# Optimization experiments

Hardware: AMD Instinct MI355X
Metric: run time of the kernel (lower is better)

The kernel has to match this reference:

```python
import jax, jax.numpy as jnp
import numpy as np

N, D, T = 4096, 256, 8
RHO = 16.0
DT = 1.0 / T


def setup_inputs() -> dict:
    key = jax.random.key(0)
    k1, k2, k3, k4 = jax.random.split(key, 4)
    X = jax.random.normal(k1, (N, D), dtype=jnp.float32)
    # learned deformation parameters (small init so the Euler flow stays stable)
    A = jax.random.normal(k2, (T, N, D), dtype=jnp.float32) * 0.01
    A_aff = jax.random.normal(k3, (T, D, D), dtype=jnp.float32) * 0.01
    b_aff = jax.random.normal(k4, (T, D), dtype=jnp.float32) * 0.01
    return {"X": X, "A": A, "A_aff": A_aff, "b_aff": b_aff}


def _flow(X, A, A_aff, b_aff):
    inv_two_rho2 = 1.0 / (2.0 * RHO * RHO)

    def step(Z, params_t):
        A_t, Aaff_t, baff_t = params_t
        # Gaussian self-kernel K[i,j] = exp(-||z_i - z_j||^2 / (2 rho^2))
        sq = jnp.sum(Z * Z, axis=1)                      # [n]
        dist = sq[:, None] + sq[None, :] - 2.0 * (Z @ Z.T)  # [n, n]
        K = jnp.exp(-dist * inv_two_rho2)
        # velocity: affine part + RKHS (kernel message aggregation) part
        v = Z @ Aaff_t.T + baff_t[None, :] + K @ A_t     # [n, d]
        return Z + DT * v, None

    Z_final, _ = jax.lax.scan(step, X, (A, A_aff, b_aff))
    return Z_final


def reference(X, A, A_aff, b_aff):
    return _flow(X, A, A_aff, b_aff)
```

## Files before the change

kernel.cpp:

```cpp
#include <hip/hip_runtime.h>


#define N_PTS 4096
#define DIM   256
#define DT_C  0.125f
#define C1    (1.0f/512.0f)

typedef __bf16 bf16x8 __attribute__((ext_vector_type(8)));
typedef float  f32x16 __attribute__((ext_vector_type(16)));
typedef float  f32x4v __attribute__((ext_vector_type(4)));
typedef unsigned int   u32x4 __attribute__((ext_vector_type(4)));
typedef unsigned short u16x8 __attribute__((ext_vector_type(8)));

__device__ __forceinline__ unsigned short f2bf(float f) {
  unsigned int u = __builtin_bit_cast(unsigned int, f);
  u += 0x7fffu + ((u >> 16) & 1u);
  return (unsigned short)(u >> 16);
}
__device__ __forceinline__ float bf2f(unsigned short s) {
  unsigned int u = ((unsigned int)s) << 16;
  return __builtin_bit_cast(float, u);
}

__global__ __launch_bounds__(256) void k_prep(const float* __restrict__ A,
                                              unsigned short* __restrict__ ATf) {
  __shared__ float sT[64][36];
  const int jgrp = blockIdx.x, ds = blockIdx.y, t = blockIdx.z;
  const int tid = threadIdx.x;
  const float* Ab = A + (size_t)t * N_PTS * DIM;
  {
    const int j_l = tid >> 2, dq = tid & 3;
    const float* src = Ab + (size_t)(jgrp * 64 + j_l) * DIM + ds * 32 + dq * 8;
    f32x4v v0 = *(const f32x4v*)src, v1 = *(const f32x4v*)(src + 4);
    *(f32x4v*)&sT[j_l][dq * 8] = v0;
    *(f32x4v*)&sT[j_l][dq * 8 + 4] = v1;
  }
  __syncthreads();
  const int jb_l = tid >> 6, l = tid & 63, l31 = l & 31, lhi = l >> 5;
  u16x8 o;
#pragma unroll
  for (int e = 0; e < 8; ++e) o[e] = f2bf(sT[jb_l * 16 + lhi * 8 + e][l31]);
  unsigned short* dst = ATf + (size_t)t * (8 * 256 * 64 * 8)
                      + ((size_t)(ds * 256 + jgrp * 4 + jb_l) * 64 + l) * 8;
  *(u16x8*)dst = o;
}

__global__ __launch_bounds__(256) void k_init(const float* __restrict__ X,
                                              unsigned short* __restrict__ Zf,
                                              float* __restrict__ erow) {
  const int tid = threadIdx.x;
  const int r = blockIdx.x * 8 + (tid >> 5), o = tid & 31;
  const size_t base = (size_t)r * DIM + o * 8;
  f32x4v z0 = *(const f32x4v*)(X + base), z1 = *(const f32x4v*)(X + base + 4);
  u16x8 zb; float s = 0.f;
#pragma unroll
  for (int i = 0; i < 4; ++i) { zb[i] = f2bf(z0[i]); zb[4 + i] = f2bf(z1[i]);
                                s += z0[i] * z0[i] + z1[i] * z1[i]; }
  *(u16x8*)(Zf + ((size_t)((r >> 5) * 16 + (o >> 1)) * 64 + (o & 1) * 32 + (r & 31)) * 8) = zb;
#pragma unroll
  for (int d = 16; d > 0; d >>= 1) s += __shfl_down(s, d, 32);
  if (o == 0) erow[r] = __expf(-s * C1);
}

__global__ __launch_bounds__(512, 4) void k_flash(
    const unsigned short* __restrict__ Zf, const float* __restrict__ erow,
    const unsigned short* __restrict__ ATf_t,
    const float* __restrict__ Aaff_t,
    unsigned short* __restrict__ Opart) {
  __shared__ __align__(16) unsigned short sZi[64 * 256];
  __shared__ __align__(16) unsigned short sP[2][64 * 64];

  const int tid = threadIdx.x, lane = tid & 63, wid = tid >> 6;
  const int l31 = lane & 31, lhi = lane >> 5;
  const int chunk = blockIdx.x;
  const int i0 = blockIdx.y * 64;
  const int ib = i0 >> 5;

  {
    const unsigned short* src = Zf + (size_t)ib * 8192;
#pragma unroll
    for (int p = 0; p < 4; ++p)
      *(u32x4*)(sZi + (size_t)(p * 512 + tid) * 8) =
          *(const u32x4*)(src + (size_t)(p * 512 + tid) * 8);
  }
  __syncthreads();

  if (wid < 4) {
    const int ip = wid >> 1, jh = wid & 1;
    float eI[16];
#pragma unroll
    for (int c = 0; c < 16; ++c)
      eI[c] = erow[i0 + ip * 32 + 4 * lhi + (c & 3) + 8 * (c >> 2)];

    for (int n = 0; n < 8; ++n) {
      u32x4 bv[16];
      {
        const unsigned short* bp =
            Zf + ((size_t)(chunk * 16 + n * 2 + jh) * 16 * 64 + lane) * 8;
#pragma unroll
        for (int ks = 0; ks < 16; ++ks) bv[ks] = *(const u32x4*)(bp + ks * 512);
      }
      f32x16 S;
#pragma unroll
      for (int i = 0; i < 16; ++i) S[i] = 0.f;
#pragma unroll
      for (int ks = 0; ks < 16; ++ks) {
        bf16x8 af = *(const bf16x8*)(sZi + ((size_t)(ip * 16 + ks) * 64 + lane) * 8);
        S = __builtin_amdgcn_mfma_f32_32x32x16_bf16(af, __builtin_bit_cast(bf16x8, bv[ks]), S, 0, 0, 0);
      }
      const float ej = erow[chunk * 512 + n * 64 + jh * 32 + l31];
      unsigned short* pb = sP[n & 1];
      const int blk = jh * 4 + (l31 >> 3), cl = l31 & 7;
#pragma unroll
      for (int c = 0; c < 16; ++c) {
        const int row = ip * 32 + 4 * lhi + (c & 3) + 8 * (c >> 2);
        pb[row * 64 + ((blk ^ (row & 7)) * 8) + cl] =
            f2bf(eI[c] * ej * __expf(2.f * C1 * S[c]));
      }
      __syncthreads();
    }
    __syncthreads();
  } else {
    const int cd = wid - 4;
    f32x16 O[2][2];
#pragma unroll
    for (int rs = 0; rs < 2; ++rs)
#pragma unroll
      for (int ct = 0; ct < 2; ++ct)
#pragma unroll
        for (int i = 0; i < 16; ++i) O[rs][ct][i] = 0.f;

#pragma unroll
    for (int q = 0; q < 2; ++q) {
      const int ksg = chunk * 2 + q;
      bf16x8 a[2];
#pragma unroll
      for (int rs = 0; rs < 2; ++rs)
        a[rs] = *(const bf16x8*)(sZi + ((size_t)(rs * 16 + ksg) * 64 + lane) * 8);
#pragma unroll
      for (int ct = 0; ct < 2; ++ct) {
        const int d = cd * 64 + ct * 32 + l31;
        const float* bp = Aaff_t + (size_t)d * DIM + ksg * 16 + lhi * 8;
        f32x4v f0 = *(const f32x4v*)bp, f1 = *(const f32x4v*)(bp + 4);
        u16x8 tb;
#pragma unroll
        for (int i = 0; i < 4; ++i) { tb[i] = f2bf(f0[i]); tb[4 + i] = f2bf(f1[i]); }
        bf16x8 bv = __builtin_bit_cast(bf16x8, tb);
#pragma unroll
        for (int rs = 0; rs < 2; ++rs)
          O[rs][ct] = __builtin_amdgcn_mfma_f32_32x32x16_bf16(a[rs], bv, O[rs][ct], 0, 0, 0);
      }
    }
    __syncthreads();

    for (int n = 1; n <= 8; ++n) {
      const int m = n - 1;
      u32x4 bw[8];
#pragma unroll
      for (int ks = 0; ks < 4; ++ks)
#pragma unroll
        for (int ct = 0; ct < 2; ++ct)
          bw[ks * 2 + ct] = *(const u32x4*)(ATf_t +
              ((size_t)((cd * 2 + ct) * 256 + chunk * 32 + m * 4 + ks) * 64 + lane) * 8);
      const unsigned short* pb = sP[m & 1];
#pragma unroll
      for (int ks = 0; ks < 4; ++ks) {
        bf16x8 a[2];
        const int blk = ks * 2 + lhi;
#pragma unroll
        for (int rs = 0; rs < 2; ++rs) {
          const int row = rs * 32 + l31;
          a[rs] = *(const bf16x8*)&pb[row * 64 + ((blk ^ (row & 7)) * 8)];
        }
#pragma unroll
        for (int rs = 0; rs < 2; ++rs)
#pragma unroll
          for (int ct = 0; ct < 2; ++ct)
            O[rs][ct] = __builtin_amdgcn_mfma_f32_32x32x16_bf16(
                a[rs], __builtin_bit_cast(bf16x8, bw[ks * 2 + ct]), O[rs][ct], 0, 0, 0);
      }
      __syncthreads();
    }

    unsigned short* ob = Opart + (size_t)chunk * N_PTS * DIM + (size_t)cd * 64 + l31;
#pragma unroll
    for (int rs = 0; rs < 2; ++rs)
#pragma unroll
      for (int c = 0; c < 16; ++c) {
        const int row = i0 + rs * 32 + 4 * lhi + (c & 3) + 8 * (c >> 2);
        ob[(size_t)row * DIM]      = f2bf(O[rs][0][c]);
        ob[(size_t)row * DIM + 32] = f2bf(O[rs][1][c]);
      }
  }
}

__global__ __launch_bounds__(256) void k_update(const float* __restrict__ Zin,
                                                const unsigned short* __restrict__ Opart,
                                                const float* __restrict__ baff_t,
                                                float* __restrict__ Zout,
                                                unsigned short* __restrict__ Zf,
                                                float* __restrict__ erow) {
  const int tid = threadIdx.x;
  const int r = blockIdx.x * 8 + (tid >> 5), o = tid & 31;
  const size_t base = (size_t)r * DIM + o * 8;
  f32x4v z0 = *(const f32x4v*)(Zin + base), z1 = *(const f32x4v*)(Zin + base + 4);
  f32x4v s0 = *(const f32x4v*)(baff_t + o * 8), s1 = *(const f32x4v*)(baff_t + o * 8 + 4);
#pragma unroll
  for (int c = 0; c < 8; ++c) {
    u16x8 p = *(const u16x8*)(Opart + (size_t)c * N_PTS * DIM + base);
#pragma unroll
    for (int i = 0; i < 4; ++i) { s0[i] += bf2f(p[i]); s1[i] += bf2f(p[4 + i]); }
  }
  u16x8 zb; float sv = 0.f;
#pragma unroll
  for (int i = 0; i < 4; ++i) {
    z0[i] += DT_C * s0[i]; z1[i] += DT_C * s1[i];
    zb[i] = f2bf(z0[i]); zb[4 + i] = f2bf(z1[i]);
    sv += z0[i] * z0[i] + z1[i] * z1[i];
  }
  *(f32x4v*)(Zout + base) = z0;
  *(f32x4v*)(Zout + base + 4) = z1;
  *(u16x8*)(Zf + ((size_t)((r >> 5) * 16 + (o >> 1)) * 64 + (o & 1) * 32 + (r & 31)) * 8) = zb;
#pragma unroll
  for (int d = 16; d > 0; d >>= 1) sv += __shfl_down(sv, d, 32);
  if (o == 0) erow[r] = __expf(-sv * C1);
}

extern "C" void kernel_launch(void* const* d_in, const int* in_sizes, int n_in,
                              void* d_out, int out_size, void* d_ws, size_t ws_size,
                              hipStream_t stream) {
  const float* X    = (const float*)d_in[0];
  const float* A    = (const float*)d_in[1];
  const float* Aaff = (const float*)d_in[2];
  const float* baff = (const float*)d_in[3];
  float* out = (float*)d_out;

  char* w = (char*)d_ws;
  size_t off = 0;
  unsigned short* ATf = (unsigned short*)(w + off); off += (size_t)8 * 8 * 256 * 64 * 8 * 2;
  unsigned short* Zf  = (unsigned short*)(w + off); off += (size_t)N_PTS * DIM * 2;
  float* erow = (float*)(w + off); off += (size_t)N_PTS * 4;
  float* Zf32 = (float*)(w + off); off += (size_t)N_PTS * DIM * 4;
  unsigned short* Opart = (unsigned short*)(w + off); off += (size_t)8 * N_PTS * DIM * 2;
  (void)ws_size; (void)in_sizes; (void)n_in; (void)out_size;

  k_prep<<<dim3(64, 8, 8), 256, 0, stream>>>(A, ATf);
  k_init<<<512, 256, 0, stream>>>(X, Zf, erow);

  const float* zin = X;
  for (int t = 0; t < 8; ++t) {
    float* zout = (t == 7) ? out : Zf32;
    k_flash<<<dim3(8, 64), 512, 0, stream>>>(
        Zf, erow, ATf + (size_t)t * (8 * 256 * 64 * 8), Aaff + (size_t)t * DIM * DIM, Opart);
    k_update<<<512, 256, 0, stream>>>(zin, Opart, baff + (size_t)t * DIM, zout, Zf, erow);
    zin = zout;
  }
}
```

Measured before the change: 381.0 us.

## Shrink flash blocks to 32 rows with one producer and two consumer waves

Reworks k_flash from 64-row tiles with 8 waves (4 producing kernel tiles, 4 accumulating) to 32-row tiles with 3 waves: one wave builds the 32x64 P tile and two waves each accumulate 128 output columns. The grid doubles to 1024 blocks and shared memory per block roughly halves, aiming for more resident blocks and better load balance across CUs. The trade-off is that each j-tile of Z and each ATf tile is reloaded by twice as many blocks. The single producer wave also serializes the S computation, so the pipeline between producer and consumers may become imbalanced.

```diff
diff --git a/kernel.cpp b/kernel.cpp
--- a/kernel.cpp
+++ b/kernel.cpp
@@ -62,134 +62,129 @@
   if (o == 0) erow[r] = __expf(-s * C1);
 }
 
-__global__ __launch_bounds__(512, 4) void k_flash(
+__global__ __launch_bounds__(192, 4) void k_flash(
     const unsigned short* __restrict__ Zf, const float* __restrict__ erow,
     const unsigned short* __restrict__ ATf_t,
     const float* __restrict__ Aaff_t,
     unsigned short* __restrict__ Opart) {
-  __shared__ __align__(16) unsigned short sZi[64 * 256];
-  __shared__ __align__(16) unsigned short sP[2][64 * 64];
+  __shared__ __align__(16) unsigned short sZi[16 * 64 * 8];
+  __shared__ __align__(16) unsigned short sP[2][32 * 64];
 
   const int tid = threadIdx.x, lane = tid & 63, wid = tid >> 6;
   const int l31 = lane & 31, lhi = lane >> 5;
   const int chunk = blockIdx.x;
-  const int i0 = blockIdx.y * 64;
-  const int ib = i0 >> 5;
+  const int iblk = blockIdx.y;
+  const int i0 = iblk * 32;
 
   {
-    const unsigned short* src = Zf + (size_t)ib * 8192;
-#pragma unroll
-    for (int p = 0; p < 4; ++p)
-      *(u32x4*)(sZi + (size_t)(p * 512 + tid) * 8) =
-          *(const u32x4*)(src + (size_t)(p * 512 + tid) * 8);
+    const unsigned short* src = Zf + (size_t)iblk * 8192;
+#pragma unroll
+    for (int p = 0; p < 6; ++p) {
+      int idx = p * 192 + tid;
+      if (idx < 1024)
+        *(u32x4*)(sZi + (size_t)idx * 8) = *(const u32x4*)(src + (size_t)idx * 8);
+    }
   }
   __syncthreads();
 
-  if (wid < 4) {
-    const int ip = wid >> 1, jh = wid & 1;
+  if (wid == 0) {
     float eI[16];
 #pragma unroll
     for (int c = 0; c < 16; ++c)
-      eI[c] = erow[i0 + ip * 32 + 4 * lhi + (c & 3) + 8 * (c >> 2)];
+      eI[c] = erow[i0 + 4 * lhi + (c & 3) + 8 * (c >> 2)];
 
     for (int n = 0; n < 8; ++n) {
-      u32x4 bv[16];
-      {
-        const unsigned short* bp =
-            Zf + ((size_t)(chunk * 16 + n * 2 + jh) * 16 * 64 + lane) * 8;
-#pragma unroll
-        for (int ks = 0; ks < 16; ++ks) bv[ks] = *(const u32x4*)(bp + ks * 512);
-      }
-      f32x16 S;
-#pragma unroll
-      for (int i = 0; i < 16; ++i) S[i] = 0.f;
-#pragma unroll
-      for (int ks = 0; ks < 16; ++ks) {
-        bf16x8 af = *(const bf16x8*)(sZi + ((size_t)(ip * 16 + ks) * 64 + lane) * 8);
-        S = __builtin_amdgcn_mfma_f32_32x32x16_bf16(af, __builtin_bit_cast(bf16x8, bv[ks]), S, 0, 0, 0);
-      }
-      const float ej = erow[chunk * 512 + n * 64 + jh * 32 + l31];
       unsigned short* pb = sP[n & 1];
-      const int blk = jh * 4 + (l31 >> 3), cl = l31 & 7;
-#pragma unroll
-      for (int c = 0; c < 16; ++c) {
-        const int row = ip * 32 + 4 * lhi + (c & 3) + 8 * (c >> 2);
-        pb[row * 64 + ((blk ^ (row & 7)) * 8) + cl] =
-            f2bf(eI[c] * ej * __expf(2.f * C1 * S[c]));
+#pragma unroll
+      for (int jh = 0; jh < 2; ++jh) {
+        u32x4 bv[16];
+        {
+          const unsigned short* bp =
+              Zf + ((size_t)(chunk * 16 + n * 2 + jh) * 16 * 64 + lane) * 8;
+#pragma unroll
+          for (int ks = 0; ks < 16; ++ks) bv[ks] = *(const u32x4*)(bp + ks * 512);
+        }
+        f32x16 S;
+#pragma unroll
+        for (int i = 0; i < 16; ++i) S[i] = 0.f;
+#pragma unroll
+        for (int ks = 0; ks < 16; ++ks) {
+          bf16x8 af = *(const bf16x8*)(sZi + ((size_t)ks * 64 + lane) * 8);
+          S = __builtin_amdgcn_mfma_f32_32x32x16_bf16(
+              af, __builtin_bit_cast(bf16x8, bv[ks]), S, 0, 0, 0);
+        }
+        const float ej = erow[chunk * 512 + n * 64 + jh * 32 + l31];
+        const int blk = jh * 4 + (l31 >> 3), cl = l31 & 7;
+#pragma unroll
+        for (int c = 0; c < 16; ++c) {
+          const int row = 4 * lhi + (c & 3) + 8 * (c >> 2);
+          pb[row * 64 + ((blk ^ (row & 7)) * 8) + cl] =
+              f2bf(eI[c] * ej * __expf(2.f * C1 * S[c]));
+        }
       }
       __syncthreads();
     }
     __syncthreads();
   } else {
-    const int cd = wid - 4;
-    f32x16 O[2][2];
-#pragma unroll
-    for (int rs = 0; rs < 2; ++rs)
-#pragma unroll
-      for (int ct = 0; ct < 2; ++ct)
-#pragma unroll
-        for (int i = 0; i < 16; ++i) O[rs][ct][i] = 0.f;
+    const int cd = wid - 1;
+    f32x16 O[4];
+#pragma unroll
+    for (int ct = 0; ct < 4; ++ct)
+#pragma unroll
+      for (int i = 0; i < 16; ++i) O[ct][i] = 0.f;
 
 #pragma unroll
     for (int q = 0; q < 2; ++q) {
       const int ksg = chunk * 2 + q;
-      bf16x8 a[2];
-#pragma unroll
-      for (int rs = 0; rs < 2; ++rs)
-        a[rs] = *(const bf16x8*)(sZi + ((size_t)(rs * 16 + ksg) * 64 + lane) * 8);
-#pragma unroll
-      for (int ct = 0; ct < 2; ++ct) {
-        const int d = cd * 64 + ct * 32 + l31;
+      bf16x8 a = *(const bf16x8*)(sZi + ((size_t)ksg * 64 + lane) * 8);
+#pragma unroll
+      for (int ct = 0; ct < 4; ++ct) {
+        const int d = (cd * 4 + ct) * 32 + l31;
         const float* bp = Aaff_t + (size_t)d * DIM + ksg * 16 + lhi * 8;
         f32x4v f0 = *(const f32x4v*)bp, f1 = *(const f32x4v*)(bp + 4);
         u16x8 tb;
 #pragma unroll
         for (int i = 0; i < 4; ++i) { tb[i] = f2bf(f0[i]); tb[4 + i] = f2bf(f1[i]); }
-        bf16x8 bv = __builtin_bit_cast(bf16x8, tb);
-#pragma unroll
-        for (int rs = 0; rs < 2; ++rs)
-          O[rs][ct] = __builtin_amdgcn_mfma_f32_32x32x16_bf16(a[rs], bv, O[rs][ct], 0, 0, 0);
+        O[ct] = __builtin_amdgcn_mfma_f32_32x32x16_bf16(
+            a, __builtin_bit_cast(bf16x8, tb), O[ct], 0, 0, 0);
       }
     }
     __syncthreads();
 
     for (int n = 1; n <= 8; ++n) {
       const int m = n - 1;
-      u32x4 bw[8];
-#pragma unroll
-      for (int ks = 0; ks < 4; ++ks)
-#pragma unroll
-        for (int ct = 0; ct < 2; ++ct)
-          bw[ks * 2 + ct] = *(const u32x4*)(ATf_t +
-              ((size_t)((cd * 2 + ct) * 256 + chunk * 32 + m * 4 + ks) * 64 + lane) * 8);
       const unsigned short* pb = sP[m & 1];
 #pragma unroll
-      for (int ks = 0; ks < 4; ++ks) {
-        bf16x8 a[2];
-        const int blk = ks * 2 + lhi;
-#pragma unroll
-        for (int rs = 0; rs < 2; ++rs) {
-          const int row = rs * 32 + l31;
-          a[rs] = *(const bf16x8*)&pb[row * 64 + ((blk ^ (row & 7)) * 8)];
-        }
-#pragma unroll
-        for (int rs = 0; rs < 2; ++rs)
-#pragma unroll
-          for (int ct = 0; ct < 2; ++ct)
-            O[rs][ct] = __builtin_amdgcn_mfma_f32_32x32x16_bf16(
-                a[rs], __builtin_bit_cast(bf16x8, bw[ks * 2 + ct]), O[rs][ct], 0, 0, 0);
+      for (int ksp = 0; ksp < 2; ++ksp) {
+        u32x4 bw[8];
+#pragma unroll
+        for (int k2 = 0; k2 < 2; ++k2)
+#pragma unroll
+          for (int ct = 0; ct < 4; ++ct)
+            bw[k2 * 4 + ct] = *(const u32x4*)(ATf_t +
+                ((size_t)((cd * 4 + ct) * 256 + chunk * 32 + m * 4 + ksp * 2 + k2) * 64 + lane) * 8);
+#pragma unroll
+        for (int k2 = 0; k2 < 2; ++k2) {
+          const int ks = ksp * 2 + k2;
+          const int blk = ks * 2 + lhi;
+          const int row = l31;
+          bf16x8 a = *(const bf16x8*)&pb[row * 64 + ((blk ^ (row & 7)) * 8)];
+#pragma unroll
+          for (int ct = 0; ct < 4; ++ct)
+            O[ct] = __builtin_amdgcn_mfma_f32_32x32x16_bf16(
+                a, __builtin_bit_cast(bf16x8, bw[k2 * 4 + ct]), O[ct], 0, 0, 0);
+        }
       }
       __syncthreads();
     }
 
-    unsigned short* ob = Opart + (size_t)chunk * N_PTS * DIM + (size_t)cd * 64 + l31;
-#pragma unroll
-    for (int rs = 0; rs < 2; ++rs)
+    unsigned short* ob = Opart + (size_t)chunk * N_PTS * DIM + (size_t)cd * 128 + l31;
+#pragma unroll
+    for (int ct = 0; ct < 4; ++ct)
 #pragma unroll
       for (int c = 0; c < 16; ++c) {
-        const int row = i0 + rs * 32 + 4 * lhi + (c & 3) + 8 * (c >> 2);
-        ob[(size_t)row * DIM]      = f2bf(O[rs][0][c]);
-        ob[(size_t)row * DIM + 32] = f2bf(O[rs][1][c]);
+        const int row = i0 + 4 * lhi + (c & 3) + 8 * (c >> 2);
+        ob[(size_t)row * DIM + ct * 32] = f2bf(O[ct][c]);
       }
   }
 }
@@ -250,7 +245,7 @@
   const float* zin = X;
   for (int t = 0; t < 8; ++t) {
     float* zout = (t == 7) ? out : Zf32;
-    k_flash<<<dim3(8, 64), 512, 0, stream>>>(
+    k_flash<<<dim3(8, 128), 192, 0, stream>>>(
         Zf, erow, ATf + (size_t)t * (8 * 256 * 64 * 8), Aaff + (size_t)t * DIM * DIM, Opart);
     k_update<<<512, 256, 0, stream>>>(zin, Opart, baff + (size_t)t * DIM, zout, Zf, erow);
     zin = zout;
```

Measured after the change: 448.1 us. +17.6%, slower.
